# Kernel optimization log

Measured on AMD Instinct MI355X. Metric: run time of the kernel, lower is better.

Reference implementation:

```python
import jax, jax.numpy as jnp
import numpy as np

M_POW = 4   # m: number of visual-graph powers
N_POW = 4   # n: number of text-graph powers
T = 32      # temporal length, forced by torch.eye(32) in GraphFusion
EPS_BN = 1e-5


def conv1d_same(x, w, b):
    # x: (B, Cin, L), w: (Cout, Cin, 3) -> (B, Cout, L), padding=1
    y = jax.lax.conv_general_dilated(x, w, window_strides=(1,), padding=[(1, 1)],
                                     dimension_numbers=("NCH", "OIH", "NCH"))
    return y + b[None, :, None]


def setup_inputs() -> dict:
    key = jax.random.key(0)
    ks = jax.random.split(key, 10)
    b, c = 128, 5
    d = {}
    d["v_feature"] = jax.random.normal(ks[0], (b, c, T, 2048), jnp.float32)
    d["t_feature"] = jax.random.normal(ks[1], (b, c, T, 768), jnp.float32)
    # Temporal embedding convs (Conv1d k=3, pad=1)
    d["wv"] = jax.random.normal(ks[2], (32, 2048, 3), jnp.float32) * 0.02
    d["bv"] = jnp.zeros((32,), jnp.float32)
    d["wt"] = jax.random.normal(ks[3], (32, 768, 3), jnp.float32) * 0.02
    d["bt"] = jnp.zeros((32,), jnp.float32)
    # GraphFusion learned (m, n) bilinear matrix: torch.normal(0, 1)
    d["fusion_a"] = jax.random.normal(ks[4], (M_POW, N_POW), jnp.float32)
    # NormalHead (BN-WVAD style, in_channel=32, hidden 2 -> 1 -> 1, all k=1 convs)
    d["w1"] = jax.random.normal(ks[5], (2, 32), jnp.float32) * 0.1
    d["b1"] = jnp.zeros((2,), jnp.float32)
    d["g1"] = jnp.ones((2,), jnp.float32)
    d["be1"] = jnp.zeros((2,), jnp.float32)
    d["w2"] = jax.random.normal(ks[6], (1, 2), jnp.float32) * 0.1
    d["b2"] = jnp.zeros((1,), jnp.float32)
    d["g2"] = jnp.ones((1,), jnp.float32)
    d["be2"] = jnp.zeros((1,), jnp.float32)
    d["w3"] = jax.random.normal(ks[7], (1, 1), jnp.float32) * 0.1
    d["b3"] = jnp.zeros((1,), jnp.float32)
    return d


def _forward(v_feature, t_feature, wv, bv, wt, bt, fusion_a,
             w1, b1, g1, be1, w2, b2, g2, be2, w3, b3):
    b, c, t, feat_v = v_feature.shape
    B = b * c
    fv = v_feature.reshape(B, t, feat_v)
    ft = t_feature.reshape(B, t, t_feature.shape[3])
    # Temporal: permute -> conv1d(k=3,pad=1) -> relu -> permute
    fv = jax.nn.relu(conv1d_same(fv.transpose(0, 2, 1), wv, bv)).transpose(0, 2, 1)  # (B,t,32)
    ft = jax.nn.relu(conv1d_same(ft.transpose(0, 2, 1), wt, bt)).transpose(0, 2, 1)  # (B,t,32)

    # GraphFusion
    def l2n(x):
        return x / jnp.maximum(jnp.linalg.norm(x, axis=2, keepdims=True), 1e-12)
    f_v = l2n(fv)
    f_t = l2n(ft)
    a_v = jax.nn.relu(jnp.einsum('bid,bjd->bij', f_v, f_v))  # (B,t,t)
    a_t = jax.nn.relu(jnp.einsum('bid,bjd->bij', f_t, f_t))  # (B,t,t)
    eye = jnp.broadcast_to(jnp.eye(t, dtype=a_v.dtype), (B, t, t))
    # power 0 replaced by identity, as in the torch code
    av_p = jnp.stack([eye] + [a_v ** i for i in range(1, M_POW)], axis=0)  # (m,B,t,t)
    at_p = jnp.stack([eye] + [a_t ** j for j in range(1, N_POW)], axis=0)  # (n,B,t,t)
    # einsum('bijk,kl,blij->bij') with the permutes undone == 'kbij,kl,lbij->bij'
    a_fused = jnp.einsum('kbij,kl,lbij->bij', av_p, fusion_a, at_p)
    a_fused = jax.nn.relu(a_fused)
    a_fused = a_fused / (jnp.max(a_fused) + 0.01)

    # NormalHead on x = a_fused.permute(0,2,1) : (B, C=t, L=t)
    x = a_fused.transpose(0, 2, 1)

    def bn(h, g, beta):  # training-mode BatchNorm1d over (N, L) per channel
        mu = h.mean(axis=(0, 2), keepdims=True)
        var = h.var(axis=(0, 2), keepdims=True)
        return (h - mu) * jax.lax.rsqrt(var + EPS_BN) * g[None, :, None] + beta[None, :, None]

    x1 = jnp.einsum('oc,bcl->bol', w1, x) + b1[None, :, None]
    h1 = jax.nn.relu(bn(x1, g1, be1))
    x2 = jnp.einsum('oc,bcl->bol', w2, h1) + b2[None, :, None]
    h2 = jax.nn.relu(bn(x2, g2, be2))
    scores = jax.nn.sigmoid(jnp.einsum('oc,bcl->bol', w3, h2) + b3[None, :, None])  # (B,1,t)
    normal_scores = scores.reshape(b, c, t).mean(axis=1)  # (b, t), crop-averaged
    return (normal_scores, a_v, a_t, a_fused)


def reference(v_feature, t_feature, wv, bv, wt, bt, fusion_a,
              w1, b1, g1, be1, w2, b2, g2, be2, w3, b3):
    return _forward(v_feature, t_feature, wv, bv, wt, bt, fusion_a,
                    w1, b1, g1, be1, w2, b2, g2, be2, w3, b3)
```

## Files before the change

kernel.cpp:

```cpp
#include <hip/hip_runtime.h>
#include <hip/hip_bf16.h>
#include <math.h>


typedef __attribute__((ext_vector_type(8))) short short8;
typedef __attribute__((ext_vector_type(4))) float f32x4;

#define XROW 132

__device__ __forceinline__ unsigned short f2bf(float f) {
    __hip_bfloat16 h = __float2bfloat16(f);
    return *reinterpret_cast<unsigned short*>(&h);
}
__device__ __forceinline__ float bf2f(unsigned short u) {
    return __uint_as_float(((unsigned int)u) << 16);
}
__device__ __forceinline__ short8 lds_frag(const unsigned short* p) {
    union { uint2 u2[2]; short8 s; } r;
    r.u2[0] = *reinterpret_cast<const uint2*>(p);
    r.u2[1] = *reinterpret_cast<const uint2*>(p + 4);
    return r.s;
}
__device__ __forceinline__ short8 glb_frag(const unsigned short* p) {
    union { uint4 u; short8 s; } r;
    r.u = *reinterpret_cast<const uint4*>(p);
    return r.s;
}

__global__ __launch_bounds__(256) void pack_kernel(
    const float* __restrict__ wv, const float* __restrict__ wt,
    unsigned short* __restrict__ wvpk, unsigned short* __restrict__ wtpk,
    float* __restrict__ scal) {
    int gid = blockIdx.x * 256 + threadIdx.x;
    if (gid < 16) scal[gid] = 0.f;
    const int NV = 196608, NT = 73728;
    if (gid < NV) {
        int o = gid / 6144, rem = gid % 6144;
        int c = rem / 3, k = rem % 3;
        int s = c >> 5, cp = c & 31;
        float f = wv[gid];
        unsigned short h = f2bf(f);
        unsigned short l = f2bf(f - bf2f(h));
        int base = (s * 3 + k) * 2048 + o * 32 + cp;
        wvpk[base] = h;
        wvpk[base + 1024] = l;
    } else if (gid < NV + NT) {
        int g = gid - NV;
        int o = g / 2304, rem = g % 2304;
        int c = rem / 3, k = rem % 3;
        int s = c >> 5, cp = c & 31;
        float f = wt[g];
        unsigned short h = f2bf(f);
        unsigned short l = f2bf(f - bf2f(h));
        int base = (s * 3 + k) * 2048 + o * 32 + cp;
        wtpk[base] = h;
        wtpk[base + 1024] = l;
    }
}

__device__ __forceinline__ void conv_phase(
    const float* __restrict__ xb, int Cin,
    const unsigned short* __restrict__ wpk,
    unsigned short* hiT, unsigned short* loT,
    float* __restrict__ yout, int tid, int wave, int lane) {
    __syncthreads();
    if (tid < XROW) {
        hiT[tid] = 0; hiT[33 * XROW + tid] = 0;
        loT[tid] = 0; loT[33 * XROW + tid] = 0;
    }
    f32x4 acc0 = {0.f, 0.f, 0.f, 0.f};
    f32x4 acc1 = {0.f, 0.f, 0.f, 0.f};
    int tm = wave & 1, tn = wave >> 1;
    int m = lane & 15, quad = lane >> 4;
    int c4 = tid & 31, tg = tid >> 5;
    int nchunk = Cin >> 7;
    for (int ch = 0; ch < nchunk; ++ch) {
        int c0 = ch << 7;
        __syncthreads();
#pragma unroll
        for (int pass = 0; pass < 4; ++pass) {
            int t = tg + (pass << 3);
            const float4 xq = *reinterpret_cast<const float4*>(
                xb + (size_t)t * Cin + c0 + (c4 << 2));
            unsigned short h0 = f2bf(xq.x), h1 = f2bf(xq.y);
            unsigned short h2 = f2bf(xq.z), h3 = f2bf(xq.w);
            unsigned short l0 = f2bf(xq.x - bf2f(h0));
            unsigned short l1 = f2bf(xq.y - bf2f(h1));
            unsigned short l2 = f2bf(xq.z - bf2f(h2));
            unsigned short l3 = f2bf(xq.w - bf2f(h3));
            int widx = (t + 1) * XROW + (c4 << 2);
            *reinterpret_cast<uint2*>(hiT + widx) =
                make_uint2(h0 | ((unsigned int)h1 << 16), h2 | ((unsigned int)h3 << 16));
            *reinterpret_cast<uint2*>(loT + widx) =
                make_uint2(l0 | ((unsigned int)l1 << 16), l2 | ((unsigned int)l3 << 16));
        }
        __syncthreads();
        int sbase = c0 >> 5;
        int arow0 = (tm << 4) + m;
        int bofs = ((tn << 4) + m) * 32 + (quad << 3);
#pragma unroll
        for (int sl = 0; sl < 4; ++sl) {
            int acol = (sl << 5) + (quad << 3);
            const unsigned short* bbase = wpk + (size_t)(sbase + sl) * 6144 + bofs;
#pragma unroll
            for (int k = 0; k < 3; ++k) {
                short8 Ah = lds_frag(hiT + (arow0 + k) * XROW + acol);
                short8 Al = lds_frag(loT + (arow0 + k) * XROW + acol);
                short8 Bh = glb_frag(bbase + k * 2048);
                short8 Bl = glb_frag(bbase + k * 2048 + 1024);
                acc0 = __builtin_amdgcn_mfma_f32_16x16x32_bf16(Ah, Bh, acc0, 0, 0, 0);
                acc1 = __builtin_amdgcn_mfma_f32_16x16x32_bf16(Ah, Bl, acc1, 0, 0, 0);
                acc1 = __builtin_amdgcn_mfma_f32_16x16x32_bf16(Al, Bh, acc1, 0, 0, 0);
            }
        }
    }
    int ocol = (tn << 4) + m;
#pragma unroll
    for (int r = 0; r < 4; ++r) {
        int t = (tm << 4) + (quad << 2) + r;
        yout[t * 32 + ocol] = acc0[r] + acc1[r];
    }
}

__global__ __launch_bounds__(256, 4) void conv_mfma_kernel(
    const float* __restrict__ xv, const unsigned short* __restrict__ wvpk,
    const float* __restrict__ xt, const unsigned short* __restrict__ wtpk,
    float* __restrict__ yv, float* __restrict__ yt) {
    __shared__ unsigned short hiT[34 * XROW], loT[34 * XROW];
    int b = blockIdx.x, tid = threadIdx.x;
    int wave = tid >> 6, lane = tid & 63;
    conv_phase(xv + (size_t)b * 32 * 2048, 2048, wvpk, hiT, loT,
               yv + (size_t)b * 1024, tid, wave, lane);
    conv_phase(xt + (size_t)b * 32 * 768, 768, wtpk, hiT, loT,
               yt + (size_t)b * 1024, tid, wave, lane);
}

__global__ __launch_bounds__(256) void s2_kernel(
    const float* __restrict__ fvp, const float* __restrict__ ftp,
    const float* __restrict__ bv, const float* __restrict__ bt,
    const float* __restrict__ fuse, float* __restrict__ out_av,
    float* __restrict__ out_at, float* __restrict__ out_af,
    unsigned int* __restrict__ maxslot) {
    int b = blockIdx.x, tid = threadIdx.x;
    __shared__ float Fv[32][33], Ft[32][33], inv[64], wmax[4];
#pragma unroll
    for (int e = 0; e < 4; ++e) {
        int idx = tid + 256 * e;
        int i = idx >> 5, j = idx & 31;
        Fv[i][j] = fmaxf(fvp[b * 1024 + idx] + bv[j], 0.f);
        Ft[i][j] = fmaxf(ftp[b * 1024 + idx] + bt[j], 0.f);
    }
    __syncthreads();
    {
        int row = tid >> 3, cg = (tid & 7) * 4;
        float sv = 0.f, st = 0.f;
#pragma unroll
        for (int q = 0; q < 4; ++q) {
            float v = Fv[row][cg + q]; sv = fmaf(v, v, sv);
            float u = Ft[row][cg + q]; st = fmaf(u, u, st);
        }
        sv += __shfl_xor(sv, 1); sv += __shfl_xor(sv, 2); sv += __shfl_xor(sv, 4);
        st += __shfl_xor(st, 1); st += __shfl_xor(st, 2); st += __shfl_xor(st, 4);
        if ((tid & 7) == 0) {
            inv[row]      = rsqrtf(fmaxf(sv, 1e-24f));
            inv[32 + row] = rsqrtf(fmaxf(st, 1e-24f));
        }
    }
    __syncthreads();
    float fa[16];
#pragma unroll
    for (int q = 0; q < 16; ++q) fa[q] = fuse[q];
    float lmax = 0.f;
#pragma unroll
    for (int e = 0; e < 4; ++e) {
        int idx = tid + 256 * e;
        int i = idx >> 5, j = idx & 31;
        float dv = 0.f, dt_ = 0.f;
        for (int c = 0; c < 32; ++c) {
            dv  = fmaf(Fv[i][c], Fv[j][c], dv);
            dt_ = fmaf(Ft[i][c], Ft[j][c], dt_);
        }
        float av = fmaxf(dv  * inv[i] * inv[j], 0.f);
        float at = fmaxf(dt_ * inv[32 + i] * inv[32 + j], 0.f);
        out_av[b * 1024 + idx] = av;
        out_at[b * 1024 + idx] = at;
        float pv0 = (i == j) ? 1.f : 0.f;
        float pv1 = av, pv2 = av * av, pv3 = pv2 * av;
        float pt1 = at, pt2 = at * at, pt3 = pt2 * at;
        float af = 0.f;
        af += (fa[0] * pv0 + fa[4] * pv1 + fa[8]  * pv2 + fa[12] * pv3) * pv0;
        af += (fa[1] * pv0 + fa[5] * pv1 + fa[9]  * pv2 + fa[13] * pv3) * pt1;
        af += (fa[2] * pv0 + fa[6] * pv1 + fa[10] * pv2 + fa[14] * pv3) * pt2;
        af += (fa[3] * pv0 + fa[7] * pv1 + fa[11] * pv2 + fa[15] * pv3) * pt3;
        float r = fmaxf(af, 0.f);
        out_af[b * 1024 + idx] = r;
        lmax = fmaxf(lmax, r);
    }
    for (int off = 1; off < 64; off <<= 1)
        lmax = fmaxf(lmax, __shfl_xor(lmax, off));
    if ((tid & 63) == 0) wmax[tid >> 6] = lmax;
    __syncthreads();
    if (tid == 0) {
        float mx = fmaxf(fmaxf(wmax[0], wmax[1]), fmaxf(wmax[2], wmax[3]));
        atomicMax(maxslot, __float_as_uint(mx));
    }
}

__global__ __launch_bounds__(256) void s3_kernel(
    float* __restrict__ af, const float* __restrict__ w1,
    const float* __restrict__ b1, float* __restrict__ x1,
    float* __restrict__ scal) {
    int b = blockIdx.x, tid = threadIdx.x;
    __shared__ float A[32][33];
    float inv = 1.0f / (__uint_as_float(((const unsigned int*)scal)[0]) + 0.01f);
#pragma unroll
    for (int e = 0; e < 4; ++e) {
        int idx = tid + 256 * e;
        float v = af[b * 1024 + idx] * inv;
        af[b * 1024 + idx] = v;
        A[idx >> 5][idx & 31] = v;
    }
    __syncthreads();
    if (tid < 64) {
        int o = tid >> 5, l = tid & 31;
        float s = b1[o];
        for (int c = 0; c < 32; ++c) s = fmaf(w1[o * 32 + c], A[l][c], s);
        x1[(size_t)(b * 2 + o) * 32 + l] = s;
        float s1 = s, s2 = s * s;
        for (int off = 1; off < 32; off <<= 1) {
            s1 += __shfl_xor(s1, off);
            s2 += __shfl_xor(s2, off);
        }
        if (l == 0) {
            atomicAdd(&scal[1 + o], s1);
            atomicAdd(&scal[3 + o], s2);
        }
    }
}

__global__ __launch_bounds__(256) void s4_kernel(
    const float* __restrict__ x1, const float* __restrict__ g1,
    const float* __restrict__ be1, const float* __restrict__ w2,
    const float* __restrict__ b2, float* __restrict__ x2,
    float* __restrict__ scal) {
    int idx = blockIdx.x * 256 + threadIdx.x;
    const float N = 20480.f;
    float mu0 = scal[1] / N, mu1 = scal[2] / N;
    float va0 = scal[3] / N - mu0 * mu0, va1 = scal[4] / N - mu1 * mu1;
    float rs0 = rsqrtf(va0 + 1e-5f), rs1 = rsqrtf(va1 + 1e-5f);
    int b = idx >> 5, l = idx & 31;
    float h0 = fmaxf((x1[(size_t)(b * 2 + 0) * 32 + l] - mu0) * rs0 * g1[0] + be1[0], 0.f);
    float h1 = fmaxf((x1[(size_t)(b * 2 + 1) * 32 + l] - mu1) * rs1 * g1[1] + be1[1], 0.f);
    float v = w2[0] * h0 + w2[1] * h1 + b2[0];
    x2[idx] = v;
    float s1 = v, s2 = v * v;
    for (int off = 1; off < 64; off <<= 1) {
        s1 += __shfl_xor(s1, off);
        s2 += __shfl_xor(s2, off);
    }
    __shared__ float ps[4][2];
    int lane = threadIdx.x & 63, w = threadIdx.x >> 6;
    if (lane == 0) { ps[w][0] = s1; ps[w][1] = s2; }
    __syncthreads();
    if (threadIdx.x == 0) {
        atomicAdd(&scal[5], ps[0][0] + ps[1][0] + ps[2][0] + ps[3][0]);
        atomicAdd(&scal[6], ps[0][1] + ps[1][1] + ps[2][1] + ps[3][1]);
    }
}

__global__ __launch_bounds__(256) void s5_kernel(
    const float* __restrict__ x2, const float* __restrict__ g2,
    const float* __restrict__ be2, const float* __restrict__ w3,
    const float* __restrict__ b3, float* __restrict__ ns,
    const float* __restrict__ scal) {
    int idx = blockIdx.x * 256 + threadIdx.x;
    const float N = 20480.f;
    float mu = scal[5] / N;
    float var = scal[6] / N - mu * mu;
    float rs = rsqrtf(var + 1e-5f);
    int bb = idx >> 5, t = idx & 31;
    float s = 0.f;
#pragma unroll
    for (int crop = 0; crop < 5; ++crop) {
        int b = bb * 5 + crop;
        float h = fmaxf((x2[b * 32 + t] - mu) * rs * g2[0] + be2[0], 0.f);
        float z = w3[0] * h + b3[0];
        s += 1.f / (1.f + expf(-z));
    }
    ns[idx] = s * 0.2f;
}

extern "C" void kernel_launch(void* const* d_in, const int* in_sizes, int n_in,
                              void* d_out, int out_size, void* d_ws, size_t ws_size,
                              hipStream_t stream) {
    const float* v_feat = (const float*)d_in[0];
    const float* t_feat = (const float*)d_in[1];
    const float* wv  = (const float*)d_in[2];
    const float* bv  = (const float*)d_in[3];
    const float* wt  = (const float*)d_in[4];
    const float* bt  = (const float*)d_in[5];
    const float* fuse= (const float*)d_in[6];
    const float* w1  = (const float*)d_in[7];
    const float* b1  = (const float*)d_in[8];
    const float* g1  = (const float*)d_in[9];
    const float* be1 = (const float*)d_in[10];
    const float* w2  = (const float*)d_in[11];
    const float* b2  = (const float*)d_in[12];
    const float* g2  = (const float*)d_in[13];
    const float* be2 = (const float*)d_in[14];
    const float* w3  = (const float*)d_in[15];
    const float* b3  = (const float*)d_in[16];

    float* ws   = (float*)d_ws;
    float* scal = ws;
    unsigned short* wvpk = (unsigned short*)(ws + 16);
    unsigned short* wtpk = (unsigned short*)(ws + 16 + 196608);
    float* fv   = ws + 16 + 196608 + 73728;
    float* ft   = fv + 655360;
    float* x1   = ft + 655360;
    float* x2   = x1 + 40960;

    float* out_ns = (float*)d_out;
    float* out_av = out_ns + 4096;
    float* out_at = out_av + 655360;
    float* out_af = out_at + 655360;

    pack_kernel<<<1056, 256, 0, stream>>>(wv, wt, wvpk, wtpk, scal);
    conv_mfma_kernel<<<640, 256, 0, stream>>>(v_feat, wvpk, t_feat, wtpk, fv, ft);
    s2_kernel<<<640, 256, 0, stream>>>(fv, ft, bv, bt, fuse, out_av, out_at,
                                       out_af, (unsigned int*)scal);
    s3_kernel<<<640, 256, 0, stream>>>(out_af, w1, b1, x1, scal);
    s4_kernel<<<80, 256, 0, stream>>>(x1, g1, be1, w2, b2, x2, scal);
    s5_kernel<<<16, 256, 0, stream>>>(x2, g2, be2, w3, b3, out_ns, scal);
}
```

Baseline: 396.4 us.

## Split conv input-channel reduction across blocks with atomic accumulation

The conv kernel now splits each sample's input-channel reduction into chunks handled by separate blocks: four per sample for the visual features and two per sample for the text features, giving 3840 blocks instead of 640. Partial sums are combined with atomicAdd into output buffers that the pack kernel now zeroes first. This raises parallelism and occupancy (launch bounds go to 8 blocks per CU) so the memory-bound streaming of the large feature tensors uses more of the GPU. In exchange it adds float atomics, extra zeroing traffic and a summation order that is no longer deterministic.

```diff
diff --git a/kernel.cpp b/kernel.cpp
--- a/kernel.cpp
+++ b/kernel.cpp
@@ -30,9 +30,10 @@
 __global__ __launch_bounds__(256) void pack_kernel(
     const float* __restrict__ wv, const float* __restrict__ wt,
     unsigned short* __restrict__ wvpk, unsigned short* __restrict__ wtpk,
-    float* __restrict__ scal) {
+    float* __restrict__ scal, float* __restrict__ zbuf, int nz) {
     int gid = blockIdx.x * 256 + threadIdx.x;
     if (gid < 16) scal[gid] = 0.f;
+    for (int i = gid; i < nz; i += gridDim.x * 256) zbuf[i] = 0.f;
     const int NV = 196608, NT = 73728;
     if (gid < NV) {
         int o = gid / 6144, rem = gid % 6144;
@@ -58,12 +59,23 @@
     }
 }
 
-__device__ __forceinline__ void conv_phase(
-    const float* __restrict__ xb, int Cin,
-    const unsigned short* __restrict__ wpk,
-    unsigned short* hiT, unsigned short* loT,
-    float* __restrict__ yout, int tid, int wave, int lane) {
-    __syncthreads();
+__global__ __launch_bounds__(256, 8) void conv_mfma_kernel(
+    const float* __restrict__ xv, const unsigned short* __restrict__ wvpk,
+    const float* __restrict__ xt, const unsigned short* __restrict__ wtpk,
+    float* __restrict__ yv, float* __restrict__ yt) {
+    __shared__ unsigned short hiT[34 * XROW], loT[34 * XROW];
+    int bid = blockIdx.x;
+    const float* x; const unsigned short* wpk; float* y;
+    int Cin, b, c0g, nchunk;
+    if (bid < 2560) {
+        x = xv; wpk = wvpk; y = yv; Cin = 2048;
+        b = bid >> 2; c0g = (bid & 3) << 9; nchunk = 4;
+    } else {
+        int tb = bid - 2560;
+        x = xt; wpk = wtpk; y = yt; Cin = 768;
+        b = tb >> 1; c0g = (tb & 1) * 384; nchunk = 3;
+    }
+    int tid = threadIdx.x, wave = tid >> 6, lane = tid & 63;
     if (tid < XROW) {
         hiT[tid] = 0; hiT[33 * XROW + tid] = 0;
         loT[tid] = 0; loT[33 * XROW + tid] = 0;
@@ -73,10 +85,10 @@
     int tm = wave & 1, tn = wave >> 1;
     int m = lane & 15, quad = lane >> 4;
     int c4 = tid & 31, tg = tid >> 5;
-    int nchunk = Cin >> 7;
+    const float* xb = x + (size_t)b * 32 * Cin + c0g;
     for (int ch = 0; ch < nchunk; ++ch) {
         int c0 = ch << 7;
-        __syncthreads();
+        if (ch) __syncthreads();
 #pragma unroll
         for (int pass = 0; pass < 4; ++pass) {
             int t = tg + (pass << 3);
@@ -95,7 +107,7 @@
                 make_uint2(l0 | ((unsigned int)l1 << 16), l2 | ((unsigned int)l3 << 16));
         }
         __syncthreads();
-        int sbase = c0 >> 5;
+        int sbase = (c0g + c0) >> 5;
         int arow0 = (tm << 4) + m;
         int bofs = ((tn << 4) + m) * 32 + (quad << 3);
 #pragma unroll
@@ -118,21 +130,8 @@
 #pragma unroll
     for (int r = 0; r < 4; ++r) {
         int t = (tm << 4) + (quad << 2) + r;
-        yout[t * 32 + ocol] = acc0[r] + acc1[r];
-    }
-}
-
-__global__ __launch_bounds__(256, 4) void conv_mfma_kernel(
-    const float* __restrict__ xv, const unsigned short* __restrict__ wvpk,
-    const float* __restrict__ xt, const unsigned short* __restrict__ wtpk,
-    float* __restrict__ yv, float* __restrict__ yt) {
-    __shared__ unsigned short hiT[34 * XROW], loT[34 * XROW];
-    int b = blockIdx.x, tid = threadIdx.x;
-    int wave = tid >> 6, lane = tid & 63;
-    conv_phase(xv + (size_t)b * 32 * 2048, 2048, wvpk, hiT, loT,
-               yv + (size_t)b * 1024, tid, wave, lane);
-    conv_phase(xt + (size_t)b * 32 * 768, 768, wtpk, hiT, loT,
-               yt + (size_t)b * 1024, tid, wave, lane);
+        atomicAdd(&y[(size_t)b * 1024 + t * 32 + ocol], acc0[r] + acc1[r]);
+    }
 }
 
 __global__ __launch_bounds__(256) void s2_kernel(
@@ -325,8 +324,8 @@
     float* out_at = out_av + 655360;
     float* out_af = out_at + 655360;
 
-    pack_kernel<<<1056, 256, 0, stream>>>(wv, wt, wvpk, wtpk, scal);
-    conv_mfma_kernel<<<640, 256, 0, stream>>>(v_feat, wvpk, t_feat, wtpk, fv, ft);
+    pack_kernel<<<1056, 256, 0, stream>>>(wv, wt, wvpk, wtpk, scal, fv, 2 * 655360);
+    conv_mfma_kernel<<<3840, 256, 0, stream>>>(v_feat, wvpk, t_feat, wtpk, fv, ft);
     s2_kernel<<<640, 256, 0, stream>>>(fv, ft, bv, bt, fuse, out_av, out_at,
                                        out_af, (unsigned int*)scal);
     s3_kernel<<<640, 256, 0, stream>>>(out_af, w1, b1, x1, scal);
```

After: 401.6 us. About the same (+1.3%).
